# Kernel tuning notes

Hardware: AMD Instinct MI355X
Metric: run time of the kernel (lower is better)

Reference implementation:

```python
import jax, jax.numpy as jnp
import numpy as np
from jax import lax

# dims
B, T_MEL, N_MEL, L_TXT, D_TXT = 8, 400, 80, 128, 512
E, HID, EMB, N_SPK = 256, 256, 128, 100
H = HID // 2  # per-direction LSTM hidden


def setup_inputs() -> dict:
    key = jax.random.key(0)
    ks = jax.random.split(key, 16)
    def n(k, shape, s=0.02):
        return jax.random.normal(k, shape, jnp.float32) * s
    return {
        "x": n(ks[0], (B, N_MEL, T_MEL), 1.0),
        "input_lengths": jax.random.randint(ks[1], (B,), T_MEL // 2, T_MEL + 1).astype(jnp.int32),
        "text": n(ks[2], (B, L_TXT, D_TXT), 1.0),
        "text_lengths": jax.random.randint(ks[3], (B,), L_TXT // 2, L_TXT + 1).astype(jnp.int32),
        "Wx": n(ks[4], (E, N_MEL)), "bx": jnp.zeros((E,), jnp.float32),
        "Wq": n(ks[5], (E, D_TXT)), "bq": jnp.zeros((E,), jnp.float32),
        "Wout": n(ks[6], (E, E)), "bout": jnp.zeros((E,), jnp.float32),
        "v": jax.random.normal(ks[7], (E, 1), jnp.float32) * 0.1,
        "lstm_wih": n(ks[8], (2, 2, 4 * H, HID)),
        "lstm_whh": n(ks[9], (2, 2, 4 * H, H)),
        "lstm_bih": jnp.zeros((2, 2, 4 * H), jnp.float32),
        "lstm_bhh": jnp.zeros((2, 2, 4 * H), jnp.float32),
        "p1_w": n(ks[10], (EMB, HID)), "p1_b": jnp.zeros((EMB,), jnp.float32),
        "p2_w": n(ks[11], (N_SPK, EMB)), "p2_b": jnp.zeros((N_SPK,), jnp.float32),
    }


def _run_lstm(x, Wih, Whh, bih, bhh):
    # x: [B, L, in] -> outputs [B, L, H]; PyTorch gate order i,f,g,o
    h0 = jnp.zeros((x.shape[0], Whh.shape[1]), x.dtype)
    c0 = jnp.zeros_like(h0)
    def step(carry, xt):
        h, c = carry
        g = xt @ Wih.T + h @ Whh.T + (bih + bhh)
        i, f, gg, o = jnp.split(g, 4, axis=-1)
        c = jax.nn.sigmoid(f) * c + jax.nn.sigmoid(i) * jnp.tanh(gg)
        h = jax.nn.sigmoid(o) * jnp.tanh(c)
        return (h, c), h
    _, hs = lax.scan(step, (h0, c0), x.swapaxes(0, 1))  # scan over time
    return hs.swapaxes(0, 1)


def _reverse_by_length(x, lengths):
    # reverse the first lengths[b] steps of each sequence (pack_padded semantics)
    L = x.shape[1]
    idx = jnp.clip(lengths[:, None] - 1 - jnp.arange(L)[None, :], 0, L - 1)
    return jnp.take_along_axis(x, idx[:, :, None], axis=1)


def reference(x, input_lengths, text, text_lengths, Wx, bx, Wq, bq, Wout, bout, v,
              lstm_wih, lstm_whh, lstm_bih, lstm_bhh, p1_w, p1_b, p2_w, p2_b):
    # ---- vectorized VanillaAttention over all text tokens ----
    mels = x.swapaxes(1, 2)                       # [B, T, M]
    x1 = mels @ Wx.T + bx                         # [B, T, E]   linear_x
    q1 = text @ Wq.T + bq                         # [B, L, E]   linear_q
    # v^T @ out_linear(tanh(.)) == tanh(.) @ (Wout^T v) + v . bout
    w = Wout.T @ v[:, 0]                          # [E]
    c = bout @ v[:, 0]                            # scalar
    s = jnp.tanh(x1[:, None, :, :] + q1[:, :, None, :])   # [B, L, T, E]
    scores = jnp.einsum('blte,e->blt', s, w) + c           # [B, L, T]
    mel_mask = jnp.arange(T_MEL)[None, :] < input_lengths[:, None]   # [B, T]
    scores = jnp.where(mel_mask[:, None, :], scores, -jnp.inf)
    scores = jax.nn.softmax(scores, axis=-1)
    contexts = jnp.einsum('blt,bte->ble', scores, x1)       # [B, L, E]
    h = q1 + contexts                                       # LSTM input

    # ---- 2-layer bidirectional LSTM (packed semantics via per-length reversal) ----
    for layer in range(2):
        fwd = _run_lstm(h, lstm_wih[layer, 0], lstm_whh[layer, 0], lstm_bih[layer, 0], lstm_bhh[layer, 0])
        rev = _reverse_by_length(h, text_lengths)
        bwd = _run_lstm(rev, lstm_wih[layer, 1], lstm_whh[layer, 1], lstm_bih[layer, 1], lstm_bhh[layer, 1])
        bwd = _reverse_by_length(bwd, text_lengths)
        h = jnp.concatenate([fwd, bwd], axis=-1)            # [B, L, HID]

    # ---- masked mean pool (pad_packed zeros the padding before the sum) ----
    txt_mask = (jnp.arange(L_TXT)[None, :] < text_lengths[:, None]).astype(h.dtype)
    pooled = (h * txt_mask[:, :, None]).sum(axis=1) / text_lengths[:, None].astype(h.dtype)

    out = jnp.tanh(pooled @ p1_w.T + p1_b)
    embeddings = out / jnp.linalg.norm(out, axis=1, keepdims=True)
    logits = out @ p2_w.T + p2_b
    return logits, embeddings, scores
```

## Files before the change

kernel.cpp:

```cpp
#include <hip/hip_runtime.h>
#include <hip/hip_bf16.h>
#include <math.h>

#define B 8
#define T_MEL 400
#define N_MEL 80
#define L_TXT 128
#define D_TXT 512
#define E 256
#define HID 256
#define EMB 128
#define N_SPK 100
#define HH 128

#define OFF_W      0
#define OFF_C      256
#define OFF_WXT    272
#define OFF_WQT    (OFF_WXT + N_MEL*E)
#define OFF_WIHT   (OFF_WQT + D_TXT*E)
#define OFF_BSUM   (OFF_WIHT + 2*2*256*512)
#define OFF_X1     (OFF_BSUM + 2048)
#define OFF_Q1     (OFF_X1 + B*T_MEL*E)
#define OFF_G      OFF_X1
#define OFF_H0     (OFF_Q1 + B*L_TXT*E)
#define OFF_O1     (OFF_H0 + B*L_TXT*E)
#define OFF_HS0    OFF_H0
#define OFF_POOL   OFF_O1
#define OFF_WG     (OFF_O1 + 4096)

typedef _Float16 half2v __attribute__((ext_vector_type(2)));

__device__ __forceinline__ float fast_sigmoid(float x){ return 1.f/(1.f+__expf(-x)); }
__device__ __forceinline__ float fast_tanh(float x){ float e=__expf(2.f*x); return 1.f - 2.f/(e+1.f); }

__device__ __forceinline__ float fdot2(uint a, uint b, float c){
  half2v ha = __builtin_bit_cast(half2v, a);
  half2v hb = __builtin_bit_cast(half2v, b);
#if __has_builtin(__builtin_amdgcn_fdot2)
  return __builtin_amdgcn_fdot2(ha, hb, c, false);
#else
  float r;
  asm("v_dot2_f32_f16 %0, %1, %2, %3" : "=v"(r) : "v"(a), "v"(b), "v"(c));
  return r;
#endif
}
__device__ __forceinline__ uint packh2(float a, float b){
  union { _Float16 h[2]; uint u; } x;
  x.h[0] = (_Float16)a; x.h[1] = (_Float16)b; return x.u;
}

__global__ __launch_bounds__(256) void k_prep(const float* __restrict__ Wout, const float* __restrict__ bout,
                       const float* __restrict__ v,    const float* __restrict__ Wx,
                       const float* __restrict__ Wq,   const float* __restrict__ wih,
                       const float* __restrict__ bih,  const float* __restrict__ bhh,
                       const float* __restrict__ whh,  float* __restrict__ ws){
  __shared__ __align__(16) float tile[64][81];
  __shared__ __align__(16) uint  utile[64][129];
  int blk = blockIdx.x, tid = threadIdx.x;
  if (blk == 0){
    float acc = 0.f;
    for (int j=0;j<E;j++) acc += Wout[j*E + tid] * v[j];
    ws[OFF_W + tid] = acc;
    if (tid==0){ float c=0.f; for(int j=0;j<E;j++) c += bout[j]*v[j]; ws[OFF_C]=c; }
  } else if (blk <= 4){
    int e0 = (blk-1)*64;
    for (int idx = tid; idx < 64*20; idx += 256){
      int e = idx/20, c4 = idx%20;
      float4 vv = *(const float4*)&Wx[(size_t)(e0+e)*N_MEL + 4*c4];
      tile[e][4*c4]=vv.x; tile[e][4*c4+1]=vv.y; tile[e][4*c4+2]=vv.z; tile[e][4*c4+3]=vv.w;
    }
    __syncthreads();
    for (int idx = tid; idx < N_MEL*64; idx += 256){
      int m = idx>>6, e = idx&63;
      ws[OFF_WXT + m*E + e0 + e] = tile[e][m];
    }
  } else if (blk <= 36){
    int t = blk-5; int e0 = (t&3)*64, k0 = (t>>2)*64;
    for (int idx = tid; idx < 64*16; idx += 256){
      int e = idx>>4, c = idx&15;
      float4 vv = *(const float4*)&Wq[(size_t)(e0+e)*D_TXT + k0 + 4*c];
      tile[e][4*c]=vv.x; tile[e][4*c+1]=vv.y; tile[e][4*c+2]=vv.z; tile[e][4*c+3]=vv.w;
    }
    __syncthreads();
    for (int idx = tid; idx < 64*64; idx += 256){
      int k = idx>>6, e = idx&63;
      ws[OFF_WQT + (k0+k)*E + e0 + e] = tile[e][k];
    }
  } else if (blk <= 68){
    int t = blk-37; int ld = t>>3, g0 = (t&7)*64;
    for (int idx = tid; idx < 64*64; idx += 256){
      int g = idx>>6, c = idx&63;
      float4 vv = *(const float4*)&wih[((size_t)(ld*512+g0+g))*256 + 4*c];
      utile[g][2*c]   = packh2(vv.x, vv.y);
      utile[g][2*c+1] = packh2(vv.z, vv.w);
    }
    __syncthreads();
    uint* wout = (uint*)(ws + OFF_WIHT) + (size_t)ld*128*512;
    for (int idx = tid; idx < 128*64; idx += 256){
      int k2 = idx>>6, g = idx&63;
      wout[(size_t)k2*512 + g0 + g] = utile[g][k2];
    }
  } else if (blk == 69){
    for (int i = tid; i < 2048; i += 256)
      ws[OFF_BSUM + i] = bih[i] + bhh[i];
  } else {
    int bp = blk - 70;
    int ld = bp >> 2, w = bp & 3;
    uint* wg = (uint*)(ws + OFF_WG) + ((size_t)ld*4 + w)*8192;
    for (int ii = 0; ii < 32; ii++){
      int i = ii*256 + tid;
      int r  = i >> 11;
      int jj = (i >> 8) & 7;
      int l  = (i >> 2) & 63;
      int k  = i & 3;
      int u  = w*32 + (l >> 1);
      int hf = l & 1;
      const float* src = whh + ((size_t)(ld*512 + r*128 + u))*HH + 64*hf + jj*8 + 2*k;
      wg[i] = packh2(src[0], src[1]);
    }
  }
}

__global__ __launch_bounds__(256) void k_xq(const float* __restrict__ x,    const float* __restrict__ bx,
                                            const float* __restrict__ text, const float* __restrict__ bq,
                                            float* __restrict__ ws){
  __shared__ float sbuf[2048];
  int blk = blockIdx.x, tid = threadIdx.x;
  if (blk < 800){
    int b = blk/100; int t0 = (blk%100)*4;
    float (*sx)[4] = (float(*)[4])sbuf;
    for (int i = tid; i < N_MEL*4; i += 256){
      int m = i>>2, ii = i&3;
      sx[m][ii] = x[(b*N_MEL+m)*T_MEL + t0 + ii];
    }
    __syncthreads();
    float bxe = bx[tid];
    float a0=bxe,a1=bxe,a2=bxe,a3=bxe;
    const float* wxt = ws + OFF_WXT;
    #pragma unroll 4
    for (int m=0;m<N_MEL;m++){
      float w = wxt[m*E + tid];
      a0 += sx[m][0]*w; a1 += sx[m][1]*w; a2 += sx[m][2]*w; a3 += sx[m][3]*w;
    }
    float* x1 = ws + OFF_X1 + (b*T_MEL + t0)*E + tid;
    x1[0]=a0; x1[E]=a1; x1[2*E]=a2; x1[3*E]=a3;
  } else {
    int bb = blk - 800;
    int b = bb/32; int l0 = (bb%32)*4;
    float (*st)[D_TXT] = (float(*)[D_TXT])sbuf;
    for (int i = tid; i < 4*D_TXT; i += 256){
      int li = i / D_TXT, k = i % D_TXT;
      st[li][k] = text[(b*L_TXT + l0 + li)*D_TXT + k];
    }
    __syncthreads();
    float bqe = bq[tid];
    float a0=bqe,a1=bqe,a2=bqe,a3=bqe;
    const float* wqt = ws + OFF_WQT;
    #pragma unroll 2
    for (int k=0;k<D_TXT;k++){
      float w = wqt[k*E + tid];
      a0 += st[0][k]*w; a1 += st[1][k]*w; a2 += st[2][k]*w; a3 += st[3][k]*w;
    }
    float* q1 = ws + OFF_Q1 + (b*L_TXT + l0)*E + tid;
    q1[0]=a0; q1[E]=a1; q1[2*E]=a2; q1[3*E]=a3;
  }
}

__global__ __launch_bounds__(256) void k_score(const int* __restrict__ mel_len,
                                               float* __restrict__ ws,
                                               float* __restrict__ d_out){
  int blk = blockIdx.x; int b = blk >> 7; int l = blk & 127;
  int tid = threadIdx.x; int lane = tid & 63; int wv = tid >> 6;
  __shared__ __align__(16) float sl[T_MEL];
  __shared__ float red[8];
  const float* x1 = ws + OFF_X1 + b*T_MEL*E;
  const float* q1 = ws + OFF_Q1 + (b*L_TXT+l)*E;
  int g = lane >> 4, i = lane & 15;
  float qv[16], wvv[16];
  {
    const float4* q4 = (const float4*)(q1 + i*16);
    const float4* w4 = (const float4*)(ws + OFF_W + i*16);
    #pragma unroll
    for (int j=0;j<4;j++){
      float4 a = q4[j]; qv[4*j]=a.x; qv[4*j+1]=a.y; qv[4*j+2]=a.z; qv[4*j+3]=a.w;
      float4 c = w4[j]; wvv[4*j]=c.x; wvv[4*j+1]=c.y; wvv[4*j+2]=c.z; wvv[4*j+3]=c.w;
    }
  }
  float cc = ws[OFF_C];
  int len = mel_len[b];
  #pragma unroll 2
  for (int iter=0; iter<25; iter++){
    int t = iter*16 + wv*4 + g;
    const float4* xr = (const float4*)(x1 + t*E + i*16);
    float s = 0.f;
    #pragma unroll
    for (int j=0;j<4;j++){
      float4 xv = xr[j];
      s += wvv[4*j+0]*fast_tanh(xv.x + qv[4*j+0]);
      s += wvv[4*j+1]*fast_tanh(xv.y + qv[4*j+1]);
      s += wvv[4*j+2]*fast_tanh(xv.z + qv[4*j+2]);
      s += wvv[4*j+3]*fast_tanh(xv.w + qv[4*j+3]);
    }
    s += __shfl_xor(s,1); s += __shfl_xor(s,2);
    s += __shfl_xor(s,4); s += __shfl_xor(s,8);
    if (i==0) sl[t] = s + cc;
  }
  __syncthreads();
  float mx = -3.0e38f;
  for (int t = tid; t < T_MEL; t += 256) if (t < len) mx = fmaxf(mx, sl[t]);
  #pragma unroll
  for (int off=32; off>=1; off>>=1) mx = fmaxf(mx, __shfl_xor(mx, off));
  if (lane==0) red[wv] = mx;
  __syncthreads();
  mx = fmaxf(fmaxf(red[0],red[1]),fmaxf(red[2],red[3]));
  float se = 0.f;
  for (int t = tid; t < T_MEL; t += 256){
    float p = (t < len) ? __expf(sl[t]-mx) : 0.f;
    sl[t] = p; se += p;
  }
  #pragma unroll
  for (int off=32; off>=1; off>>=1) se += __shfl_xor(se, off);
  if (lane==0) red[4+wv] = se;
  __syncthreads();
  float rsum = 1.f/(red[4]+red[5]+red[6]+red[7]);
  float* sc_out = d_out + 1824 + (b*L_TXT + l)*T_MEL;
  for (int t = tid; t < T_MEL; t += 256){
    float p = sl[t]*rsum;
    sl[t] = p; sc_out[t] = p;
  }
  __syncthreads();
  float a = 0.f;
  int e = tid;
  for (int t = 0; t < T_MEL; t += 4){
    float4 p4 = *(const float4*)&sl[t];
    a += p4.x*x1[(t  )*E+e] + p4.y*x1[(t+1)*E+e]
       + p4.z*x1[(t+2)*E+e] + p4.w*x1[(t+3)*E+e];
  }
  ws[OFF_H0 + (b*L_TXT+l)*E + e] = q1[e] + a;
}

__global__ __launch_bounds__(512) void k_gates(const float* __restrict__ in,
                                               const float* __restrict__ hs,
                                               const int* __restrict__ txt_len,
                                               float* __restrict__ gates, int layer,
                                               float* __restrict__ ws){
  int idx = blockIdx.x; int tt = idx & 15; int dir = (idx>>4)&1; int b = idx>>5;
  int tid = threadIdx.x;
  __shared__ __align__(16) uint sih[8][128];
  int len = txt_len[b];
  for (int i = tid; i < 8*128; i += 512){
    int r = i >> 7, k2 = i & 127;
    int t = tt*8 + r;
    int row = dir ? max(0, len-1-t) : t;
    float va, vb;
    if (layer == 0){
      const float2 p = *(const float2*)&in[((size_t)(b*L_TXT + row))*HID + 2*k2];
      va = p.x; vb = p.y;
    } else {
      int k = 2*k2; int d = k >> 7, u = k & 127;
      int sidx = (d==0) ? row : (row < len ? len-1-row : 0);
      const float2 p = *(const float2*)&hs[(((size_t)d*L_TXT + sidx)*8 + b)*128 + u];
      va = p.x; vb = p.y;
    }
    sih[r][k2] = packh2(va, vb);
  }
  __syncthreads();
  int ld = layer*2 + dir;
  int g = tid;
  float bsum = ws[OFF_BSUM + ld*512 + g];
  float acc[8];
  #pragma unroll
  for (int r=0;r<8;r++) acc[r] = bsum;
  const uint* wt2 = (const uint*)(ws + OFF_WIHT) + (size_t)ld*128*512 + g;
  for (int k4=0; k4<128; k4+=4){
    uint w0 = wt2[(k4  )*512];
    uint w1 = wt2[(k4+1)*512];
    uint w2 = wt2[(k4+2)*512];
    uint w3 = wt2[(k4+3)*512];
    #pragma unroll
    for (int r=0;r<8;r++){
      uint4 s4 = *(const uint4*)&sih[r][k4];
      acc[r] = fdot2(s4.x, w0, acc[r]);
      acc[r] = fdot2(s4.y, w1, acc[r]);
      acc[r] = fdot2(s4.z, w2, acc[r]);
      acc[r] = fdot2(s4.w, w3, acc[r]);
    }
  }
  float* go = gates + (((size_t)(dir*L_TXT + tt*8)*8) + b)*512 + g;
  #pragma unroll
  for (int r=0;r<8;r++) go[(size_t)r*8*512] = acc[r];
}

__global__ __launch_bounds__(256) void k_scan(const float* __restrict__ Gp,
                                              const float* __restrict__ whh_all,
                                              const uint* __restrict__ wg,
                                              const int* __restrict__ txt_len,
                                              float* __restrict__ hseq,
                                              float* __restrict__ pooled, int layer){
  int dir = blockIdx.x & 1; int b = blockIdx.x >> 1;
  int tid = threadIdx.x;
  int l = tid & 63, w = tid >> 6;
  int u  = tid >> 1;
  int hf = tid & 1;

  __shared__ uint wlds[24576];
  __shared__ uint h2buf[2][64];

  const float* wbase = whh_all + (size_t)(layer*2+dir)*512*HH;
  #pragma unroll
  for (int r=0;r<2;r++){
    const float* wr = wbase + (size_t)(r*128+u)*HH + 64*hf;
    #pragma unroll
    for (int jj=0;jj<8;jj++){
      uint4 vv;
      vv.x = packh2(wr[jj*8+0], wr[jj*8+1]);
      vv.y = packh2(wr[jj*8+2], wr[jj*8+3]);
      vv.z = packh2(wr[jj*8+4], wr[jj*8+5]);
      vv.w = packh2(wr[jj*8+6], wr[jj*8+7]);
      *(uint4*)(wlds + w*4096 + (r*8+jj)*256 + l*4) = vv;
    }
  }
  if (tid < 128) ((uint*)h2buf)[tid] = 0;
  int len = txt_len[b];
  bool pool = (layer == 1);

  const uint* wgp = wg + (((size_t)(layer*2+dir))*4 + w)*8192 + l*4;
  uint4 wg2[8], wg3[8];
  #pragma unroll
  for (int jj=0;jj<8;jj++){
    wg2[jj] = *(const uint4*)(wgp + (16+jj)*256);
    wg3[jj] = *(const uint4*)(wgp + (24+jj)*256);
  }
  #pragma unroll
  for (int jj=0;jj<8;jj++){
    asm volatile("" : "+v"(wg2[jj].x), "+v"(wg2[jj].y), "+v"(wg2[jj].z), "+v"(wg2[jj].w));
    asm volatile("" : "+v"(wg3[jj].x), "+v"(wg3[jj].y), "+v"(wg3[jj].z), "+v"(wg3[jj].w));
  }

  const float* gb = Gp + ((size_t)(dir*L_TXT)*8 + b)*512 + u;
  float g0 = gb[0], g1 = gb[128], g2 = gb[256], g3 = gb[384];
  float c_reg = 0.f, psum = 0.f;
  __syncthreads();

  const uint4* wp = (const uint4*)(wlds + w*4096 + l*4);

  for (int s=0; s<L_TXT; s++){
    const float* gn = gb + (size_t)(s+1 < L_TXT ? s+1 : s)*4096;
    float n0 = gn[0], n1 = gn[128], n2 = gn[256], n3 = gn[384];
    const uint4* hp = (const uint4*)(h2buf[s&1] + hf*32);
    float a0 = hf ? 0.f : g0;
    float a1 = hf ? 0.f : g1;
    float a2 = hf ? 0.f : g2;
    float a3 = hf ? 0.f : g3;
    #pragma unroll
    for (int jj=0;jj<8;jj++){
      uint4 hv = hp[jj];
      uint4 w0 = wp[(jj   )*64];
      uint4 w1 = wp[( 8+jj)*64];
      uint4 w2 = wg2[jj];
      uint4 w3 = wg3[jj];
      a0 = fdot2(w0.x,hv.x,a0); a0 = fdot2(w0.y,hv.y,a0);
      a0 = fdot2(w0.z,hv.z,a0); a0 = fdot2(w0.w,hv.w,a0);
      a1 = fdot2(w1.x,hv.x,a1); a1 = fdot2(w1.y,hv.y,a1);
      a1 = fdot2(w1.z,hv.z,a1); a1 = fdot2(w1.w,hv.w,a1);
      a2 = fdot2(w2.x,hv.x,a2); a2 = fdot2(w2.y,hv.y,a2);
      a2 = fdot2(w2.z,hv.z,a2); a2 = fdot2(w2.w,hv.w,a2);
      a3 = fdot2(w3.x,hv.x,a3); a3 = fdot2(w3.y,hv.y,a3);
      a3 = fdot2(w3.z,hv.z,a3); a3 = fdot2(w3.w,hv.w,a3);
    }
    a0 += __shfl_xor(a0, 1);
    a1 += __shfl_xor(a1, 1);
    a2 += __shfl_xor(a2, 1);
    a3 += __shfl_xor(a3, 1);
    float i_ = fast_sigmoid(a0);
    float f_ = fast_sigmoid(a1);
    float g_ = fast_tanh   (a2);
    float o_ = fast_sigmoid(a3);
    c_reg = f_*c_reg + i_*g_;
    float h = o_*fast_tanh(c_reg);
    float hn = __shfl_xor(h, 2);
    if (hf==0 && !(u&1)) h2buf[(s+1)&1][u>>1] = packh2(h, hn);
    if (pool){
      if (s < len) psum += h;
    } else {
      if (hf==0) hseq[(((size_t)dir*L_TXT + s)*8 + b)*128 + u] = h;
    }
    g0 = n0; g1 = n1; g2 = n2; g3 = n3;
    __syncthreads();
  }
  if (pool && hf==0) pooled[((size_t)(dir*8+b))*128 + u] = psum;
}

__global__ __launch_bounds__(256) void k_final(const float* __restrict__ pooled,
                                               const int* __restrict__ txt_len,
                                               const float* __restrict__ p1w,
                                               const float* __restrict__ p1b,
                                               const float* __restrict__ p2w,
                                               const float* __restrict__ p2b,
                                               float* __restrict__ d_out){
  int b = blockIdx.x; int tid = threadIdx.x;
  __shared__ float pl[HID];
  __shared__ float ol[EMB];
  __shared__ float nrm;
  int len = txt_len[b];
  int d = tid >> 7, u = tid & 127;
  pl[tid] = pooled[((size_t)(d*8+b))*128 + u] / (float)len;
  __syncthreads();
  if (tid < EMB){
    float a = p1b[tid];
    for (int k=0;k<HID;k++) a += pl[k]*p1w[tid*HID+k];
    ol[tid] = fast_tanh(a);
  }
  __syncthreads();
  if (tid == 0){
    float q = 0.f;
    for (int k=0;k<EMB;k++) q += ol[k]*ol[k];
    nrm = rsqrtf(q);
  }
  __syncthreads();
  if (tid < EMB) d_out[800 + b*EMB + tid] = ol[tid]*nrm;
  if (tid < N_SPK){
    float a = p2b[tid];
    for (int k=0;k<EMB;k++) a += ol[k]*p2w[tid*EMB+k];
    d_out[b*N_SPK + tid] = a;
  }
}

extern "C" void kernel_launch(void* const* d_in, const int* in_sizes, int n_in,
                              void* d_out, int out_size, void* d_ws, size_t ws_size,
                              hipStream_t stream) {
  const float* x       = (const float*)d_in[0];
  const int*   mel_len = (const int*)  d_in[1];
  const float* text    = (const float*)d_in[2];
  const int*   txt_len = (const int*)  d_in[3];
  const float* Wx      = (const float*)d_in[4];
  const float* bx      = (const float*)d_in[5];
  const float* Wq      = (const float*)d_in[6];
  const float* bq      = (const float*)d_in[7];
  const float* Wout    = (const float*)d_in[8];
  const float* bout    = (const float*)d_in[9];
  const float* v       = (const float*)d_in[10];
  const float* wih     = (const float*)d_in[11];
  const float* whh     = (const float*)d_in[12];
  const float* bih     = (const float*)d_in[13];
  const float* bhh     = (const float*)d_in[14];
  const float* p1w     = (const float*)d_in[15];
  const float* p1b     = (const float*)d_in[16];
  const float* p2w     = (const float*)d_in[17];
  const float* p2b     = (const float*)d_in[18];
  float* ws  = (float*)d_ws;
  float* out = (float*)d_out;
  const uint* wg = (const uint*)(ws + OFF_WG);

  k_prep <<<86, 256, 0, stream>>>(Wout, bout, v, Wx, Wq, wih, bih, bhh, whh, ws);
  k_xq   <<<1056, 256, 0, stream>>>(x, bx, text, bq, ws);
  k_score<<<1024, 256, 0, stream>>>(mel_len, ws, out);

  float* G = ws + OFF_G;
  k_gates<<<256, 512, 0, stream>>>(ws + OFF_H0, ws + OFF_HS0, txt_len, G, 0, ws);
  k_scan <<<16, 256, 0, stream>>>(G, whh, wg, txt_len, ws + OFF_HS0, ws + OFF_POOL, 0);
  k_gates<<<256, 512, 0, stream>>>(ws + OFF_H0, ws + OFF_HS0, txt_len, G, 1, ws);
  k_scan <<<16, 256, 0, stream>>>(G, whh, wg, txt_len, ws + OFF_HS0, ws + OFF_POOL, 1);

  k_final<<<8, 256, 0, stream>>>(ws + OFF_POOL, txt_len, p1w, p1b, p2w, p2b, out);
}
```

Measured before the change: 425.8 us.

## Process four text queries per score block and interleave gate layout for scan

The attention score kernel now handles four query rows per block, so each x1 tile loaded from memory is reused for four tanh-score rows and four context accumulations, and the block count drops from 1024 to 256. Softmax is done per wavefront, one query row each. The launch also requests about 78 KB of dynamic shared memory that is never used, which caps blocks per CU, apparently to force a particular occupancy. Separately, the gates buffer is written with the four gates of each hidden unit interleaved, so the sequential scan can fetch them with one float4 load per step instead of four scalar loads.

```diff
diff --git a/kernel.cpp b/kernel.cpp
--- a/kernel.cpp
+++ b/kernel.cpp
@@ -169,74 +169,101 @@
 __global__ __launch_bounds__(256) void k_score(const int* __restrict__ mel_len,
                                                float* __restrict__ ws,
                                                float* __restrict__ d_out){
-  int blk = blockIdx.x; int b = blk >> 7; int l = blk & 127;
+  extern __shared__ float dyn_pad[];
+  int blk = blockIdx.x; int b = blk >> 5; int l0 = (blk & 31)*4;
   int tid = threadIdx.x; int lane = tid & 63; int wv = tid >> 6;
-  __shared__ __align__(16) float sl[T_MEL];
-  __shared__ float red[8];
+  __shared__ __align__(16) float sl[4][T_MEL];
   const float* x1 = ws + OFF_X1 + b*T_MEL*E;
-  const float* q1 = ws + OFF_Q1 + (b*L_TXT+l)*E;
+  const float* q1b = ws + OFF_Q1 + (b*L_TXT+l0)*E;
   int g = lane >> 4, i = lane & 15;
-  float qv[16], wvv[16];
+  float qv[4][16], wvv[16];
+  #pragma unroll
+  for (int l=0;l<4;l++){
+    const float4* q4 = (const float4*)(q1b + l*E + i*16);
+    #pragma unroll
+    for (int j=0;j<4;j++){
+      float4 a = q4[j];
+      qv[l][4*j]=a.x; qv[l][4*j+1]=a.y; qv[l][4*j+2]=a.z; qv[l][4*j+3]=a.w;
+    }
+  }
   {
-    const float4* q4 = (const float4*)(q1 + i*16);
     const float4* w4 = (const float4*)(ws + OFF_W + i*16);
     #pragma unroll
     for (int j=0;j<4;j++){
-      float4 a = q4[j]; qv[4*j]=a.x; qv[4*j+1]=a.y; qv[4*j+2]=a.z; qv[4*j+3]=a.w;
-      float4 c = w4[j]; wvv[4*j]=c.x; wvv[4*j+1]=c.y; wvv[4*j+2]=c.z; wvv[4*j+3]=c.w;
+      float4 c = w4[j];
+      wvv[4*j]=c.x; wvv[4*j+1]=c.y; wvv[4*j+2]=c.z; wvv[4*j+3]=c.w;
     }
   }
   float cc = ws[OFF_C];
   int len = mel_len[b];
-  #pragma unroll 2
   for (int iter=0; iter<25; iter++){
     int t = iter*16 + wv*4 + g;
     const float4* xr = (const float4*)(x1 + t*E + i*16);
-    float s = 0.f;
+    float xb[16];
     #pragma unroll
     for (int j=0;j<4;j++){
       float4 xv = xr[j];
-      s += wvv[4*j+0]*fast_tanh(xv.x + qv[4*j+0]);
-      s += wvv[4*j+1]*fast_tanh(xv.y + qv[4*j+1]);
-      s += wvv[4*j+2]*fast_tanh(xv.z + qv[4*j+2]);
-      s += wvv[4*j+3]*fast_tanh(xv.w + qv[4*j+3]);
-    }
-    s += __shfl_xor(s,1); s += __shfl_xor(s,2);
-    s += __shfl_xor(s,4); s += __shfl_xor(s,8);
-    if (i==0) sl[t] = s + cc;
-  }
-  __syncthreads();
-  float mx = -3.0e38f;
-  for (int t = tid; t < T_MEL; t += 256) if (t < len) mx = fmaxf(mx, sl[t]);
-  #pragma unroll
-  for (int off=32; off>=1; off>>=1) mx = fmaxf(mx, __shfl_xor(mx, off));
-  if (lane==0) red[wv] = mx;
-  __syncthreads();
-  mx = fmaxf(fmaxf(red[0],red[1]),fmaxf(red[2],red[3]));
-  float se = 0.f;
-  for (int t = tid; t < T_MEL; t += 256){
-    float p = (t < len) ? __expf(sl[t]-mx) : 0.f;
-    sl[t] = p; se += p;
-  }
-  #pragma unroll
-  for (int off=32; off>=1; off>>=1) se += __shfl_xor(se, off);
-  if (lane==0) red[4+wv] = se;
-  __syncthreads();
-  float rsum = 1.f/(red[4]+red[5]+red[6]+red[7]);
-  float* sc_out = d_out + 1824 + (b*L_TXT + l)*T_MEL;
-  for (int t = tid; t < T_MEL; t += 256){
-    float p = sl[t]*rsum;
-    sl[t] = p; sc_out[t] = p;
-  }
-  __syncthreads();
-  float a = 0.f;
+      xb[4*j]=xv.x; xb[4*j+1]=xv.y; xb[4*j+2]=xv.z; xb[4*j+3]=xv.w;
+    }
+    float s0=0.f,s1=0.f,s2=0.f,s3=0.f;
+    #pragma unroll
+    for (int j=0;j<16;j++){
+      float xj = xb[j], wj = wvv[j];
+      s0 += wj*fast_tanh(xj + qv[0][j]);
+      s1 += wj*fast_tanh(xj + qv[1][j]);
+      s2 += wj*fast_tanh(xj + qv[2][j]);
+      s3 += wj*fast_tanh(xj + qv[3][j]);
+    }
+    #pragma unroll
+    for (int off=8; off>=1; off>>=1){
+      s0 += __shfl_xor(s0, off); s1 += __shfl_xor(s1, off);
+      s2 += __shfl_xor(s2, off); s3 += __shfl_xor(s3, off);
+    }
+    if (i==0){
+      sl[0][t]=s0+cc; sl[1][t]=s1+cc; sl[2][t]=s2+cc; sl[3][t]=s3+cc;
+    }
+  }
+  __syncthreads();
+  {
+    int l = wv;
+    float mx = -3.0e38f;
+    for (int t=lane; t<T_MEL; t+=64) if (t < len) mx = fmaxf(mx, sl[l][t]);
+    #pragma unroll
+    for (int off=32; off>=1; off>>=1) mx = fmaxf(mx, __shfl_xor(mx, off));
+    float se = 0.f;
+    for (int t=lane; t<T_MEL; t+=64){
+      float p = (t < len) ? __expf(sl[l][t]-mx) : 0.f;
+      sl[l][t] = p; se += p;
+    }
+    #pragma unroll
+    for (int off=32; off>=1; off>>=1) se += __shfl_xor(se, off);
+    float rs = 1.f/se;
+    float* sc = d_out + 1824 + (b*L_TXT + l0 + l)*T_MEL;
+    for (int t=lane; t<T_MEL; t+=64){
+      float p = sl[l][t]*rs;
+      sl[l][t] = p; sc[t] = p;
+    }
+  }
+  __syncthreads();
+  float a0=0.f,a1=0.f,a2=0.f,a3=0.f;
   int e = tid;
   for (int t = 0; t < T_MEL; t += 4){
-    float4 p4 = *(const float4*)&sl[t];
-    a += p4.x*x1[(t  )*E+e] + p4.y*x1[(t+1)*E+e]
-       + p4.z*x1[(t+2)*E+e] + p4.w*x1[(t+3)*E+e];
-  }
-  ws[OFF_H0 + (b*L_TXT+l)*E + e] = q1[e] + a;
+    float4 p0 = *(const float4*)&sl[0][t];
+    float4 p1 = *(const float4*)&sl[1][t];
+    float4 p2 = *(const float4*)&sl[2][t];
+    float4 p3 = *(const float4*)&sl[3][t];
+    float xv0 = x1[(t  )*E+e], xv1 = x1[(t+1)*E+e];
+    float xv2 = x1[(t+2)*E+e], xv3 = x1[(t+3)*E+e];
+    a0 += p0.x*xv0 + p0.y*xv1 + p0.z*xv2 + p0.w*xv3;
+    a1 += p1.x*xv0 + p1.y*xv1 + p1.z*xv2 + p1.w*xv3;
+    a2 += p2.x*xv0 + p2.y*xv1 + p2.z*xv2 + p2.w*xv3;
+    a3 += p3.x*xv0 + p3.y*xv1 + p3.z*xv2 + p3.w*xv3;
+  }
+  float* h0 = ws + OFF_H0 + (size_t)(b*L_TXT+l0)*E;
+  h0[0*E+e] = q1b[0*E+e] + a0;
+  h0[1*E+e] = q1b[1*E+e] + a1;
+  h0[2*E+e] = q1b[2*E+e] + a2;
+  h0[3*E+e] = q1b[3*E+e] + a3;
 }
 
 __global__ __launch_bounds__(512) void k_gates(const float* __restrict__ in,
@@ -286,7 +313,7 @@
       acc[r] = fdot2(s4.w, w3, acc[r]);
     }
   }
-  float* go = gates + (((size_t)(dir*L_TXT + tt*8)*8) + b)*512 + g;
+  float* go = gates + (((size_t)(dir*L_TXT + tt*8)*8) + b)*512 + ((g&127)<<2) + (g>>7);
   #pragma unroll
   for (int r=0;r<8;r++) go[(size_t)r*8*512] = acc[r];
 }
@@ -337,8 +364,8 @@
     asm volatile("" : "+v"(wg3[jj].x), "+v"(wg3[jj].y), "+v"(wg3[jj].z), "+v"(wg3[jj].w));
   }
 
-  const float* gb = Gp + ((size_t)(dir*L_TXT)*8 + b)*512 + u;
-  float g0 = gb[0], g1 = gb[128], g2 = gb[256], g3 = gb[384];
+  const float* gb = Gp + ((size_t)(dir*L_TXT)*8 + b)*512 + u*4;
+  float4 q = *(const float4*)gb;
   float c_reg = 0.f, psum = 0.f;
   __syncthreads();
 
@@ -346,12 +373,12 @@
 
   for (int s=0; s<L_TXT; s++){
     const float* gn = gb + (size_t)(s+1 < L_TXT ? s+1 : s)*4096;
-    float n0 = gn[0], n1 = gn[128], n2 = gn[256], n3 = gn[384];
+    float4 qn = *(const float4*)gn;
     const uint4* hp = (const uint4*)(h2buf[s&1] + hf*32);
-    float a0 = hf ? 0.f : g0;
-    float a1 = hf ? 0.f : g1;
-    float a2 = hf ? 0.f : g2;
-    float a3 = hf ? 0.f : g3;
+    float a0 = hf ? 0.f : q.x;
+    float a1 = hf ? 0.f : q.y;
+    float a2 = hf ? 0.f : q.z;
+    float a3 = hf ? 0.f : q.w;
     #pragma unroll
     for (int jj=0;jj<8;jj++){
       uint4 hv = hp[jj];
@@ -385,7 +412,7 @@
     } else {
       if (hf==0) hseq[(((size_t)dir*L_TXT + s)*8 + b)*128 + u] = h;
     }
-    g0 = n0; g1 = n1; g2 = n2; g3 = n3;
+    q = qn;
     __syncthreads();
   }
   if (pool && hf==0) pooled[((size_t)(dir*8+b))*128 + u] = psum;
@@ -454,7 +481,7 @@
 
   k_prep <<<86, 256, 0, stream>>>(Wout, bout, v, Wx, Wq, wih, bih, bhh, whh, ws);
   k_xq   <<<1056, 256, 0, stream>>>(x, bx, text, bq, ws);
-  k_score<<<1024, 256, 0, stream>>>(mel_len, ws, out);
+  k_score<<<256, 256, 79872, stream>>>(mel_len, ws, out);
 
   float* G = ws + OFF_G;
   k_gates<<<256, 512, 0, stream>>>(ws + OFF_H0, ws + OFF_HS0, txt_len, G, 0, ws);
```

Measured after the change: 431.2 us. No clear change (+1.3%).

## Hold all recurrent LSTM weights in registers and interleave gate layout

Applied to the files above, without the earlier changes.

The scan kernel now loads all four gate weight slices from the pre-packed fp16 buffer into VGPRs instead of staging two of them through LDS each step. This removes per-step LDS weight reads from the serial recurrence. k_gates writes its outputs through an LDS transpose so each unit's four gates sit contiguously, and the scan reads them with one float4 load per step. A large dynamic shared allocation is added, presumably to force one block per CU. The register pressure is high, and the pre-packed buffer must already hold the i/f rows in the expected layout.

```diff
diff --git a/kernel.cpp b/kernel.cpp
--- a/kernel.cpp
+++ b/kernel.cpp
@@ -247,6 +247,7 @@
   int idx = blockIdx.x; int tt = idx & 15; int dir = (idx>>4)&1; int b = idx>>5;
   int tid = threadIdx.x;
   __shared__ __align__(16) uint sih[8][128];
+  __shared__ float outb[8][512];
   int len = txt_len[b];
   for (int i = tid; i < 8*128; i += 512){
     int r = i >> 7, k2 = i & 127;
@@ -286,79 +287,69 @@
       acc[r] = fdot2(s4.w, w3, acc[r]);
     }
   }
-  float* go = gates + (((size_t)(dir*L_TXT + tt*8)*8) + b)*512 + g;
-  #pragma unroll
-  for (int r=0;r<8;r++) go[(size_t)r*8*512] = acc[r];
+  #pragma unroll
+  for (int r=0;r<8;r++) outb[r][g] = acc[r];
+  __syncthreads();
+  float* go = gates + (((size_t)(dir*L_TXT + tt*8)*8) + b)*512;
+  int src = (tid & 3)*128 + (tid >> 2);
+  #pragma unroll
+  for (int r=0;r<8;r++) go[(size_t)r*8*512 + tid] = outb[r][src];
 }
 
 __global__ __launch_bounds__(256) void k_scan(const float* __restrict__ Gp,
-                                              const float* __restrict__ whh_all,
                                               const uint* __restrict__ wg,
                                               const int* __restrict__ txt_len,
                                               float* __restrict__ hseq,
                                               float* __restrict__ pooled, int layer){
+  extern __shared__ uint dynpad[];
+  __shared__ uint h2buf[2][64];
   int dir = blockIdx.x & 1; int b = blockIdx.x >> 1;
   int tid = threadIdx.x;
   int l = tid & 63, w = tid >> 6;
   int u  = tid >> 1;
   int hf = tid & 1;
 
-  __shared__ uint wlds[24576];
-  __shared__ uint h2buf[2][64];
-
-  const float* wbase = whh_all + (size_t)(layer*2+dir)*512*HH;
-  #pragma unroll
-  for (int r=0;r<2;r++){
-    const float* wr = wbase + (size_t)(r*128+u)*HH + 64*hf;
-    #pragma unroll
-    for (int jj=0;jj<8;jj++){
-      uint4 vv;
-      vv.x = packh2(wr[jj*8+0], wr[jj*8+1]);
-      vv.y = packh2(wr[jj*8+2], wr[jj*8+3]);
-      vv.z = packh2(wr[jj*8+4], wr[jj*8+5]);
-      vv.w = packh2(wr[jj*8+6], wr[jj*8+7]);
-      *(uint4*)(wlds + w*4096 + (r*8+jj)*256 + l*4) = vv;
-    }
-  }
+  const uint* wgp = wg + (((size_t)(layer*2+dir))*4 + w)*8192 + l*4;
+  uint4 wi[8], wf[8], wgg[8], wo[8];
+  #pragma unroll
+  for (int jj=0;jj<8;jj++){
+    wi [jj] = *(const uint4*)(wgp + (jj   )*256);
+    wf [jj] = *(const uint4*)(wgp + ( 8+jj)*256);
+    wgg[jj] = *(const uint4*)(wgp + (16+jj)*256);
+    wo [jj] = *(const uint4*)(wgp + (24+jj)*256);
+  }
+  #pragma unroll
+  for (int jj=0;jj<8;jj++){
+    asm volatile("" : "+v"(wi [jj].x), "+v"(wi [jj].y), "+v"(wi [jj].z), "+v"(wi [jj].w));
+    asm volatile("" : "+v"(wf [jj].x), "+v"(wf [jj].y), "+v"(wf [jj].z), "+v"(wf [jj].w));
+    asm volatile("" : "+v"(wgg[jj].x), "+v"(wgg[jj].y), "+v"(wgg[jj].z), "+v"(wgg[jj].w));
+    asm volatile("" : "+v"(wo [jj].x), "+v"(wo [jj].y), "+v"(wo [jj].z), "+v"(wo [jj].w));
+  }
+
   if (tid < 128) ((uint*)h2buf)[tid] = 0;
   int len = txt_len[b];
   bool pool = (layer == 1);
 
-  const uint* wgp = wg + (((size_t)(layer*2+dir))*4 + w)*8192 + l*4;
-  uint4 wg2[8], wg3[8];
-  #pragma unroll
-  for (int jj=0;jj<8;jj++){
-    wg2[jj] = *(const uint4*)(wgp + (16+jj)*256);
-    wg3[jj] = *(const uint4*)(wgp + (24+jj)*256);
-  }
-  #pragma unroll
-  for (int jj=0;jj<8;jj++){
-    asm volatile("" : "+v"(wg2[jj].x), "+v"(wg2[jj].y), "+v"(wg2[jj].z), "+v"(wg2[jj].w));
-    asm volatile("" : "+v"(wg3[jj].x), "+v"(wg3[jj].y), "+v"(wg3[jj].z), "+v"(wg3[jj].w));
-  }
-
-  const float* gb = Gp + ((size_t)(dir*L_TXT)*8 + b)*512 + u;
-  float g0 = gb[0], g1 = gb[128], g2 = gb[256], g3 = gb[384];
+  const float* gb = Gp + ((size_t)(dir*L_TXT)*8 + b)*512 + u*4;
+  float4 q = *(const float4*)gb;
   float c_reg = 0.f, psum = 0.f;
   __syncthreads();
-
-  const uint4* wp = (const uint4*)(wlds + w*4096 + l*4);
 
   for (int s=0; s<L_TXT; s++){
     const float* gn = gb + (size_t)(s+1 < L_TXT ? s+1 : s)*4096;
-    float n0 = gn[0], n1 = gn[128], n2 = gn[256], n3 = gn[384];
+    float4 qn = *(const float4*)gn;
     const uint4* hp = (const uint4*)(h2buf[s&1] + hf*32);
-    float a0 = hf ? 0.f : g0;
-    float a1 = hf ? 0.f : g1;
-    float a2 = hf ? 0.f : g2;
-    float a3 = hf ? 0.f : g3;
+    float a0 = hf ? 0.f : q.x;
+    float a1 = hf ? 0.f : q.y;
+    float a2 = hf ? 0.f : q.z;
+    float a3 = hf ? 0.f : q.w;
     #pragma unroll
     for (int jj=0;jj<8;jj++){
       uint4 hv = hp[jj];
-      uint4 w0 = wp[(jj   )*64];
-      uint4 w1 = wp[( 8+jj)*64];
-      uint4 w2 = wg2[jj];
-      uint4 w3 = wg3[jj];
+      uint4 w0 = wi [jj];
+      uint4 w1 = wf [jj];
+      uint4 w2 = wgg[jj];
+      uint4 w3 = wo [jj];
       a0 = fdot2(w0.x,hv.x,a0); a0 = fdot2(w0.y,hv.y,a0);
       a0 = fdot2(w0.z,hv.z,a0); a0 = fdot2(w0.w,hv.w,a0);
       a1 = fdot2(w1.x,hv.x,a1); a1 = fdot2(w1.y,hv.y,a1);
@@ -385,7 +376,7 @@
     } else {
       if (hf==0) hseq[(((size_t)dir*L_TXT + s)*8 + b)*128 + u] = h;
     }
-    g0 = n0; g1 = n1; g2 = n2; g3 = n3;
+    q = qn;
     __syncthreads();
   }
   if (pool && hf==0) pooled[((size_t)(dir*8+b))*128 + u] = psum;
@@ -458,9 +449,9 @@
 
   float* G = ws + OFF_G;
   k_gates<<<256, 512, 0, stream>>>(ws + OFF_H0, ws + OFF_HS0, txt_len, G, 0, ws);
-  k_scan <<<16, 256, 0, stream>>>(G, whh, wg, txt_len, ws + OFF_HS0, ws + OFF_POOL, 0);
+  k_scan <<<16, 256, 86016, stream>>>(G, wg, txt_len, ws + OFF_HS0, ws + OFF_POOL, 0);
   k_gates<<<256, 512, 0, stream>>>(ws + OFF_H0, ws + OFF_HS0, txt_len, G, 1, ws);
-  k_scan <<<16, 256, 0, stream>>>(G, whh, wg, txt_len, ws + OFF_HS0, ws + OFF_POOL, 1);
+  k_scan <<<16, 256, 86016, stream>>>(G, wg, txt_len, ws + OFF_HS0, ws + OFF_POOL, 1);
 
   k_final<<<8, 256, 0, stream>>>(ws + OFF_POOL, txt_len, p1w, p1b, p2w, p2b, out);
 }
```

Result: no change. 433.8 us (+1.9%).
